# Performance work log

Hardware: AMD Instinct MI355X
Metric: run time of the kernel (lower is better)

## Reference

```python
import jax, jax.numpy as jnp
import numpy as np
import math

N = 50000       # nodes
E = 800000      # edges
C_IN = 64
C_OUT = 32
N_SH = 9        # (l_max+1)^2 with l_max=2
H = 32          # radial_hidden_dim


def spherical_harmonics(vectors):
    # vectors: [..., 3] -> [..., 9]; faithful to source incl. (x+iy).real == x
    norm = jnp.clip(jnp.linalg.norm(vectors, axis=-1, keepdims=True), 1e-8)
    d = vectors / norm
    x, y, z = d[..., 0], d[..., 1], d[..., 2]
    c00 = 0.5 / math.sqrt(math.pi)
    c1 = 0.5 * math.sqrt(3.0 / (2.0 * math.pi))
    c1z = 0.5 * math.sqrt(3.0 / math.pi)
    c2 = 0.25 * math.sqrt(15.0 / (2.0 * math.pi))
    c2z = 0.5 * math.sqrt(15.0 / (2.0 * math.pi))
    c20 = 0.25 * math.sqrt(5.0 / math.pi)
    feats = [
        c00 * jnp.ones_like(x),
        -c1 * x,                      # -0.5*sqrt(3/2pi)*(x+iy).real
        c1z * z,
        c1 * x,                       # 0.5*sqrt(3/2pi)*(x-iy).real
        c2 * (x * x - y * y),         # 0.25*sqrt(15/2pi)*((x+iy)^2).real
        -c2z * z * x,
        c20 * (2.0 * z * z - x * x - y * y),
        c2z * z * x,
        c2 * (x * x - y * y),
    ]
    return jnp.stack(feats, axis=-1)


def setup_inputs() -> dict:
    key = jax.random.key(0)
    ks = jax.random.split(key, 9)
    features = jax.random.normal(ks[0], (N, C_IN), dtype=jnp.float32)
    positions = jax.random.normal(ks[1], (N, 3), dtype=jnp.float32)
    edge_index = jax.random.randint(ks[2], (2, E), 0, N, dtype=jnp.int64)
    fan1 = N_SH + C_IN  # 73 (intended fan-in of first radial layer)
    W1 = jax.random.normal(ks[3], (fan1, H), dtype=jnp.float32) / math.sqrt(fan1)
    b1 = jnp.zeros((H,), dtype=jnp.float32)
    W2 = jax.random.normal(ks[4], (H, H), dtype=jnp.float32) / math.sqrt(H)
    b2 = jnp.zeros((H,), dtype=jnp.float32)
    W3 = jax.random.normal(ks[5], (H, N_SH * C_OUT), dtype=jnp.float32) / math.sqrt(H)
    b3 = jnp.zeros((N_SH * C_OUT,), dtype=jnp.float32)
    return {"features": features, "positions": positions, "W1": W1, "b1": b1,
            "W2": W2, "b2": b2, "W3": W3, "b3": b3, "edge_index": edge_index}


def reference(features, positions, W1, b1, W2, b2, W3, b3, edge_index):
    row, col = edge_index[0], edge_index[1]
    rel_pos = positions[row] - positions[col]                 # [E,3]
    dist = jnp.clip(jnp.linalg.norm(rel_pos, axis=-1, keepdims=True), 1e-8)
    directions = rel_pos / dist
    y_ij = spherical_harmonics(directions)                    # [E,9]
    combined = jnp.concatenate([y_ij, features[col]], axis=-1)  # [E,9+C_IN]
    h = jax.nn.silu(combined @ W1 + b1)
    h = jax.nn.silu(h @ W2 + b2)
    messages = h @ W3 + b3                                    # [E,9*C_OUT]
    msg = messages.reshape(-1, N_SH, C_OUT).sum(axis=1)       # [E,C_OUT]
    out = jax.ops.segment_sum(msg, row, num_segments=features.shape[0])
    return out
```

## Files before the change

kernel.cpp:

```cpp
#include <hip/hip_runtime.h>
#include <hip/hip_fp16.h>

#define NNODES 50000
#define NEDGES 800000
#define CIN 64
#define COUT 32
#define NSH 9
#define HDIM 32

#define NT_BLOCKS 6250
#define HIST_BLOCKS 782
#define SCAN_BLOCKS 125
#define SCAN_CHUNK 400

__device__ __forceinline__ void prep_body(
    int t, const float* __restrict__ W3, const float* __restrict__ b3,
    const float* __restrict__ W1, const float* __restrict__ b1,
    float* __restrict__ W3s, float* __restrict__ b3s, float* __restrict__ prm)
{
    if (t < HDIM * COUT) {
        int k = t >> 5, c = t & 31;
        float s = 0.f;
        #pragma unroll
        for (int q = 0; q < NSH; ++q) s += W3[k * (NSH * COUT) + q * COUT + c];
        W3s[t] = s;
    }
    if (t < COUT) {
        float s = 0.f;
        #pragma unroll
        for (int q = 0; q < NSH; ++q) s += b3[q * COUT + t];
        b3s[t] = s;
    }
    if (t < HDIM) {
        const float c00 = 0.28209479177387814f;
        const float c1  = 0.3454941494713355f;
        const float c1z = 0.4886025119029199f;
        const float c2  = 0.38627420202318958f;
        const float c2z = 0.7725484040463791f;
        const float c20 = 0.31539156525252005f;
        prm[t]       = b1[t] + c00 * W1[0 * HDIM + t];
        prm[32 + t]  = c1  * (W1[3 * HDIM + t] - W1[1 * HDIM + t]);
        prm[64 + t]  = c1z *  W1[2 * HDIM + t];
        prm[96 + t]  = c2z * (W1[7 * HDIM + t] - W1[5 * HDIM + t]);
        prm[128 + t] = c2  * (W1[4 * HDIM + t] + W1[8 * HDIM + t]);
        prm[160 + t] = c20 *  W1[6 * HDIM + t];
    }
}

__global__ void prep_w3(const float* __restrict__ W3, const float* __restrict__ b3,
                        const float* __restrict__ W1, const float* __restrict__ b1,
                        float* __restrict__ W3s, float* __restrict__ b3s,
                        float* __restrict__ prm) {
    prep_body(threadIdx.x, W3, b3, W1, b1, W3s, b3s, prm);
}

__global__ __launch_bounds__(256) void nt_hist(
    const float* __restrict__ feat, const float* __restrict__ W1,
    const int* __restrict__ ei, float* __restrict__ g1,
    int* __restrict__ cnt, int do_nt)
{
    int b = blockIdx.x;
    if (do_nt && b < NT_BLOCKS) {
        int tid = b * 256 + threadIdx.x;
        int n = tid >> 5, c = tid & 31;
        if (n < NNODES) {
            float acc = 0.f;
            const float* fr = feat + (size_t)n * CIN;
            const float* wp = W1 + NSH * HDIM + c;
            #pragma unroll 8
            for (int k = 0; k < CIN; ++k)
                acc = fmaf(fr[k], wp[k * HDIM], acc);
            g1[(size_t)n * HDIM + c] = acc;
        }
    } else {
        int hb = do_nt ? (b - NT_BLOCKS) : b;
        int e4 = (hb * 256 + threadIdx.x) * 4;
        if (e4 < NEDGES) {
            int4 r = *reinterpret_cast<const int4*>(ei + e4);
            atomicAdd(&cnt[r.x], 1);
            atomicAdd(&cnt[r.y], 1);
            atomicAdd(&cnt[r.z], 1);
            atomicAdd(&cnt[r.w], 1);
        }
    }
}

__global__ __launch_bounds__(256) void scan_bsum(const int* __restrict__ cnt,
                                                 int* __restrict__ bsum) {
    int b = blockIdx.x, t = threadIdx.x;
    int base = b * SCAN_CHUNK;
    int s = 0;
    for (int i = t; i < SCAN_CHUNK; i += 256) s += cnt[base + i];
    #pragma unroll
    for (int d = 32; d > 0; d >>= 1) s += __shfl_down(s, d);
    __shared__ int l4[4];
    if ((t & 63) == 0) l4[t >> 6] = s;
    __syncthreads();
    if (t == 0) bsum[b] = l4[0] + l4[1] + l4[2] + l4[3];
}

__global__ __launch_bounds__(1024) void scan_top_prep(
    const int* __restrict__ bsum, int* __restrict__ ebsum, int* __restrict__ off,
    const float* __restrict__ W3, const float* __restrict__ b3,
    const float* __restrict__ W1, const float* __restrict__ b1,
    float* __restrict__ W3s, float* __restrict__ b3s, float* __restrict__ prm)
{
    if (blockIdx.x == 1) {
        prep_body(threadIdx.x, W3, b3, W1, b1, W3s, b3s, prm);
        return;
    }
    __shared__ int lds[128];
    int t = threadIdx.x;
    if (t < 128) lds[t] = (t < SCAN_BLOCKS) ? bsum[t] : 0;
    __syncthreads();
    for (int d = 1; d < 128; d <<= 1) {
        int u = (t >= d && t < 128) ? lds[t - d] : 0;
        __syncthreads();
        if (t < 128) lds[t] += u;
        __syncthreads();
    }
    if (t < SCAN_BLOCKS) ebsum[t] = (t == 0) ? 0 : lds[t - 1];
    if (t == 0) off[NNODES] = NEDGES;
}

__global__ __launch_bounds__(256) void scan_offsets(const int* __restrict__ cnt,
                                                    const int* __restrict__ ebsum,
                                                    int* __restrict__ off,
                                                    int* __restrict__ cursor) {
    int b = blockIdx.x, t = threadIdx.x;
    int base = b * SCAN_CHUNK;
    __shared__ int lds[256];
    int2 c2 = make_int2(0, 0);
    if (t < SCAN_CHUNK / 2) c2 = reinterpret_cast<const int2*>(cnt + base)[t];
    int ps = c2.x + c2.y;
    lds[t] = ps;
    __syncthreads();
    for (int d = 1; d < 256; d <<= 1) {
        int u = (t >= d) ? lds[t - d] : 0;
        __syncthreads();
        lds[t] += u;
        __syncthreads();
    }
    int excl = lds[t] - ps;
    if (t < SCAN_CHUNK / 2) {
        int o = ebsum[b] + excl;
        int2 w = make_int2(o, o + c2.x);
        reinterpret_cast<int2*>(off + base)[t] = w;
        reinterpret_cast<int2*>(cursor + base)[t] = w;
    }
}

__global__ __launch_bounds__(256) void edge_compute_g1(
    const float* __restrict__ g1, const float* __restrict__ pos,
    const float* __restrict__ prm,
    const float* __restrict__ W2, const float* __restrict__ b2,
    const float* __restrict__ W3s, const float* __restrict__ b3s,
    const int* __restrict__ ei, int* __restrict__ cursor,
    unsigned int* __restrict__ msg)
{
    int e = blockIdx.x * blockDim.x + threadIdx.x;
    if (e >= NEDGES) return;
    int row = ei[e];
    int col = ei[NEDGES + e];

    int slot = atomicAdd(&cursor[row], 1);
    unsigned int* mp = msg + (size_t)slot * 16;

    float px = pos[3 * row + 0] - pos[3 * col + 0];
    float py = pos[3 * row + 1] - pos[3 * col + 1];
    float pz = pos[3 * row + 2] - pos[3 * col + 2];
    float dist = fmaxf(sqrtf(px * px + py * py + pz * pz), 1e-8f);
    float inv = 1.0f / dist;
    float dx = px * inv, dy = py * inv, dz = pz * inv;
    float n2 = fmaxf(sqrtf(dx * dx + dy * dy + dz * dz), 1e-8f);
    float i2 = 1.0f / n2;
    float x = dx * i2, y = dy * i2, z = dz * i2;

    float zx = z * x;
    float xxyy = x * x - y * y;
    float w6 = 2.f * z * z - x * x - y * y;

    const float* b1e = prm;
    const float* A = prm + 32;
    const float* B = prm + 64;
    const float* C = prm + 96;
    const float* D = prm + 128;
    const float* E = prm + 160;

    float h1[HDIM];
    const float4* g4 = reinterpret_cast<const float4*>(g1 + (size_t)col * HDIM);
    #pragma unroll
    for (int q = 0; q < 8; ++q) {
        float4 g = g4[q];
        h1[4 * q + 0] = g.x; h1[4 * q + 1] = g.y;
        h1[4 * q + 2] = g.z; h1[4 * q + 3] = g.w;
    }
    #pragma unroll
    for (int c = 0; c < HDIM; ++c) {
        float v = h1[c] + b1e[c];
        v = fmaf(x, A[c], v);
        v = fmaf(z, B[c], v);
        v = fmaf(zx, C[c], v);
        v = fmaf(xxyy, D[c], v);
        v = fmaf(w6, E[c], v);
        h1[c] = v / (1.f + __expf(-v));
    }

    float h2[HDIM];
    #pragma unroll
    for (int c = 0; c < HDIM; ++c) h2[c] = b2[c];
    for (int k = 0; k < HDIM; ++k) {
        float v = h1[k];
        #pragma unroll
        for (int c = 0; c < HDIM; ++c) h2[c] = fmaf(v, W2[k * HDIM + c], h2[c]);
    }
    #pragma unroll
    for (int c = 0; c < HDIM; ++c) {
        float v = h2[c];
        h2[c] = v / (1.f + __expf(-v));
    }

    float m[COUT];
    #pragma unroll
    for (int c = 0; c < COUT; ++c) m[c] = b3s[c];
    for (int k = 0; k < HDIM; ++k) {
        float v = h2[k];
        #pragma unroll
        for (int c = 0; c < COUT; ++c) m[c] = fmaf(v, W3s[k * COUT + c], m[c]);
    }

    uint4 pk[4];
    unsigned int* pu = reinterpret_cast<unsigned int*>(pk);
    #pragma unroll
    for (int q = 0; q < 16; ++q) {
        __half2 hh = __floats2half2_rn(m[2 * q], m[2 * q + 1]);
        pu[q] = *reinterpret_cast<unsigned int*>(&hh);
    }
    uint4* mp4 = reinterpret_cast<uint4*>(mp);
    #pragma unroll
    for (int q = 0; q < 4; ++q) mp4[q] = pk[q];
}

__global__ __launch_bounds__(256) void gather_kernel(
    const unsigned int* __restrict__ msg, const int* __restrict__ off,
    float* __restrict__ out)
{
    int node = blockIdx.x * 4 + (threadIdx.x >> 6);
    if (node >= NNODES) return;
    int lane = threadIdx.x & 63;
    int g = lane >> 4, p = lane & 15;
    int s0 = off[node], s1 = off[node + 1];
    float ax = 0.f, ay = 0.f;
    for (int s = s0 + g; s < s1; s += 4) {
        unsigned int u = msg[(size_t)s * 16 + p];
        __half2 h = *reinterpret_cast<__half2*>(&u);
        ax += __low2float(h);
        ay += __high2float(h);
    }
    ax += __shfl_xor(ax, 16); ay += __shfl_xor(ay, 16);
    ax += __shfl_xor(ax, 32); ay += __shfl_xor(ay, 32);
    if (lane < 16)
        reinterpret_cast<float2*>(out + (size_t)node * COUT)[p] = make_float2(ax, ay);
}

__global__ __launch_bounds__(256) void edge_atomic_kernel(
    const float* __restrict__ feat, const float* __restrict__ pos,
    const float* __restrict__ W1, const float* __restrict__ b1,
    const float* __restrict__ W2, const float* __restrict__ b2,
    const float* __restrict__ W3s, const float* __restrict__ b3s,
    const int* __restrict__ ei, float* __restrict__ out)
{
    int e = blockIdx.x * blockDim.x + threadIdx.x;
    if (e >= NEDGES) return;
    int row = ei[e];
    int col = ei[NEDGES + e];

    float px = pos[3 * row + 0] - pos[3 * col + 0];
    float py = pos[3 * row + 1] - pos[3 * col + 1];
    float pz = pos[3 * row + 2] - pos[3 * col + 2];
    float dist = fmaxf(sqrtf(px * px + py * py + pz * pz), 1e-8f);
    float inv = 1.0f / dist;
    float dx = px * inv, dy = py * inv, dz = pz * inv;
    float n2 = fmaxf(sqrtf(dx * dx + dy * dy + dz * dz), 1e-8f);
    float i2 = 1.0f / n2;
    float x = dx * i2, y = dy * i2, z = dz * i2;

    const float c00 = 0.28209479177387814f;
    const float c1  = 0.3454941494713355f;
    const float c1z = 0.4886025119029199f;
    const float c2  = 0.38627420202318958f;
    const float c2z = 0.7725484040463791f;
    const float c20 = 0.31539156525252005f;

    float sh[NSH];
    float xxyy = x * x - y * y;
    float zx = z * x;
    sh[0] = c00;
    sh[1] = -c1 * x;
    sh[2] = c1z * z;
    sh[3] = c1 * x;
    sh[4] = c2 * xxyy;
    sh[5] = -c2z * zx;
    sh[6] = c20 * (2.f * z * z - x * x - y * y);
    sh[7] = c2z * zx;
    sh[8] = c2 * xxyy;

    float h1[HDIM];
    #pragma unroll
    for (int c = 0; c < HDIM; ++c) h1[c] = b1[c];
    #pragma unroll
    for (int k = 0; k < NSH; ++k) {
        float v = sh[k];
        #pragma unroll
        for (int c = 0; c < HDIM; ++c) h1[c] = fmaf(v, W1[k * HDIM + c], h1[c]);
    }
    const float4* f4 = reinterpret_cast<const float4*>(feat + (size_t)col * CIN);
    for (int kk = 0; kk < CIN / 4; ++kk) {
        float4 f = f4[kk];
        const float* Wp = W1 + (NSH + kk * 4) * HDIM;
        #pragma unroll
        for (int c = 0; c < HDIM; ++c) h1[c] = fmaf(f.x, Wp[c], h1[c]);
        #pragma unroll
        for (int c = 0; c < HDIM; ++c) h1[c] = fmaf(f.y, Wp[HDIM + c], h1[c]);
        #pragma unroll
        for (int c = 0; c < HDIM; ++c) h1[c] = fmaf(f.z, Wp[2 * HDIM + c], h1[c]);
        #pragma unroll
        for (int c = 0; c < HDIM; ++c) h1[c] = fmaf(f.w, Wp[3 * HDIM + c], h1[c]);
    }
    #pragma unroll
    for (int c = 0; c < HDIM; ++c) {
        float v = h1[c];
        h1[c] = v / (1.f + __expf(-v));
    }

    float h2[HDIM];
    #pragma unroll
    for (int c = 0; c < HDIM; ++c) h2[c] = b2[c];
    for (int k = 0; k < HDIM; ++k) {
        float v = h1[k];
        #pragma unroll
        for (int c = 0; c < HDIM; ++c) h2[c] = fmaf(v, W2[k * HDIM + c], h2[c]);
    }
    #pragma unroll
    for (int c = 0; c < HDIM; ++c) {
        float v = h2[c];
        h2[c] = v / (1.f + __expf(-v));
    }

    float m[COUT];
    #pragma unroll
    for (int c = 0; c < COUT; ++c) m[c] = b3s[c];
    for (int k = 0; k < HDIM; ++k) {
        float v = h2[k];
        #pragma unroll
        for (int c = 0; c < COUT; ++c) m[c] = fmaf(v, W3s[k * COUT + c], m[c]);
    }

    float* op = out + (size_t)row * COUT;
    #pragma unroll
    for (int c = 0; c < COUT; ++c) atomicAdd(op + c, m[c]);
}

extern "C" void kernel_launch(void* const* d_in, const int* in_sizes, int n_in,
                              void* d_out, int out_size, void* d_ws, size_t ws_size,
                              hipStream_t stream) {
    const float* feat = (const float*)d_in[0];
    const float* pos  = (const float*)d_in[1];
    const float* W1   = (const float*)d_in[2];
    const float* b1   = (const float*)d_in[3];
    const float* W2   = (const float*)d_in[4];
    const float* b2   = (const float*)d_in[5];
    const float* W3   = (const float*)d_in[6];
    const float* b3   = (const float*)d_in[7];
    const int*   ei   = (const int*)d_in[8];
    float* outf = (float*)d_out;

    int* cnt    = (int*)d_ws;
    int* off    = cnt + NNODES;
    int* cursor = off + NNODES + 2;
    int* bsum   = cursor + NNODES;
    int* ebsum  = bsum + 128;
    const size_t head_ints = ((size_t)NNODES + (NNODES + 2) + NNODES + 128 + 128 + 3) & ~(size_t)3;
    float* fbase = (float*)(((int*)d_ws) + head_ints);
    float* W3s = fbase;
    float* b3s = W3s + HDIM * COUT;
    float* prm = b3s + COUT;
    const size_t head_floats = HDIM * COUT + COUT + 192;
    float* g1 = fbase + head_floats;
    unsigned int* msg = (unsigned int*)(g1 + (size_t)NNODES * HDIM);
    size_t need = (head_ints + head_floats + (size_t)NNODES * HDIM) * 4
                + (size_t)NEDGES * 16 * 4;

    if (ws_size >= need) {
        (void)hipMemsetAsync(cnt, 0, (size_t)NNODES * sizeof(int), stream);
        nt_hist<<<NT_BLOCKS + HIST_BLOCKS, 256, 0, stream>>>(feat, W1, ei, g1, cnt, 1);
        scan_bsum<<<SCAN_BLOCKS, 256, 0, stream>>>(cnt, bsum);
        scan_top_prep<<<2, 1024, 0, stream>>>(bsum, ebsum, off, W3, b3, W1, b1, W3s, b3s, prm);
        scan_offsets<<<SCAN_BLOCKS, 256, 0, stream>>>(cnt, ebsum, off, cursor);
        edge_compute_g1<<<(NEDGES + 255) / 256, 256, 0, stream>>>(
            g1, pos, prm, W2, b2, W3s, b3s, ei, cursor, msg);
        gather_kernel<<<(NNODES + 3) / 4, 256, 0, stream>>>(msg, off, outf);
    } else {
        (void)hipMemsetAsync(d_out, 0, (size_t)out_size * sizeof(float), stream);
        prep_w3<<<1, 1024, 0, stream>>>(W3, b3, W1, b1, W3s, b3s, prm);
        edge_atomic_kernel<<<(NEDGES + 255) / 256, 256, 0, stream>>>(
            feat, pos, W1, b1, W2, b2, W3s, b3s, ei, outf);
    }
}
```

Measured before the change: 160.8 us.

## Store node projection in fp16, merge scan kernels, use fast rsqrt and silu

The per-node first-layer projection is now stored as half precision, which halves the gather traffic per edge in the edge kernel. The three-kernel prefix scan is replaced by a single block that does a serial per-thread chunk scan plus an LDS scan, cutting two launches. The double normalisation becomes one hardware rsqrt, and silu uses the hardware reciprocal. These trade some precision (fp16 storage, approximate rcp and rsq) for less memory traffic and fewer ALU ops, and the serial scan in one block may be slow because its per-thread cnt reads are strided and uncoalesced.

Result: slower. 251.4 us (+56.4%).

```diff
diff --git a/kernel.cpp b/kernel.cpp
--- a/kernel.cpp
+++ b/kernel.cpp
@@ -10,8 +10,6 @@
 
 #define NT_BLOCKS 6250
 #define HIST_BLOCKS 782
-#define SCAN_BLOCKS 125
-#define SCAN_CHUNK 400
 
 __device__ __forceinline__ void prep_body(
     int t, const float* __restrict__ W3, const float* __restrict__ b3,
@@ -56,7 +54,7 @@
 
 __global__ __launch_bounds__(256) void nt_hist(
     const float* __restrict__ feat, const float* __restrict__ W1,
-    const int* __restrict__ ei, float* __restrict__ g1,
+    const int* __restrict__ ei, __half* __restrict__ g1h,
     int* __restrict__ cnt, int do_nt)
 {
     int b = blockIdx.x;
@@ -70,7 +68,7 @@
             #pragma unroll 8
             for (int k = 0; k < CIN; ++k)
                 acc = fmaf(fr[k], wp[k * HDIM], acc);
-            g1[(size_t)n * HDIM + c] = acc;
+            g1h[(size_t)n * HDIM + c] = __float2half(acc);
         }
     } else {
         int hb = do_nt ? (b - NT_BLOCKS) : b;
@@ -85,22 +83,8 @@
     }
 }
 
-__global__ __launch_bounds__(256) void scan_bsum(const int* __restrict__ cnt,
-                                                 int* __restrict__ bsum) {
-    int b = blockIdx.x, t = threadIdx.x;
-    int base = b * SCAN_CHUNK;
-    int s = 0;
-    for (int i = t; i < SCAN_CHUNK; i += 256) s += cnt[base + i];
-    #pragma unroll
-    for (int d = 32; d > 0; d >>= 1) s += __shfl_down(s, d);
-    __shared__ int l4[4];
-    if ((t & 63) == 0) l4[t >> 6] = s;
-    __syncthreads();
-    if (t == 0) bsum[b] = l4[0] + l4[1] + l4[2] + l4[3];
-}
-
-__global__ __launch_bounds__(1024) void scan_top_prep(
-    const int* __restrict__ bsum, int* __restrict__ ebsum, int* __restrict__ off,
+__global__ __launch_bounds__(1024) void scan_all(
+    const int* __restrict__ cnt, int* __restrict__ off, int* __restrict__ cursor,
     const float* __restrict__ W3, const float* __restrict__ b3,
     const float* __restrict__ W1, const float* __restrict__ b1,
     float* __restrict__ W3s, float* __restrict__ b3s, float* __restrict__ prm)
@@ -109,49 +93,35 @@
         prep_body(threadIdx.x, W3, b3, W1, b1, W3s, b3s, prm);
         return;
     }
-    __shared__ int lds[128];
+    __shared__ int lds[1024];
+    const int C = (NNODES + 1023) / 1024;
     int t = threadIdx.x;
-    if (t < 128) lds[t] = (t < SCAN_BLOCKS) ? bsum[t] : 0;
+    int begin = t * C, end = min(begin + C, NNODES);
+    int s = 0;
+    for (int i = begin; i < end; ++i) s += cnt[i];
+    lds[t] = s;
     __syncthreads();
-    for (int d = 1; d < 128; d <<= 1) {
-        int u = (t >= d && t < 128) ? lds[t - d] : 0;
+    for (int d = 1; d < 1024; d <<= 1) {
+        int v = (t >= d) ? lds[t - d] : 0;
         __syncthreads();
-        if (t < 128) lds[t] += u;
+        lds[t] += v;
         __syncthreads();
     }
-    if (t < SCAN_BLOCKS) ebsum[t] = (t == 0) ? 0 : lds[t - 1];
-    if (t == 0) off[NNODES] = NEDGES;
-}
-
-__global__ __launch_bounds__(256) void scan_offsets(const int* __restrict__ cnt,
-                                                    const int* __restrict__ ebsum,
-                                                    int* __restrict__ off,
-                                                    int* __restrict__ cursor) {
-    int b = blockIdx.x, t = threadIdx.x;
-    int base = b * SCAN_CHUNK;
-    __shared__ int lds[256];
-    int2 c2 = make_int2(0, 0);
-    if (t < SCAN_CHUNK / 2) c2 = reinterpret_cast<const int2*>(cnt + base)[t];
-    int ps = c2.x + c2.y;
-    lds[t] = ps;
-    __syncthreads();
-    for (int d = 1; d < 256; d <<= 1) {
-        int u = (t >= d) ? lds[t - d] : 0;
-        __syncthreads();
-        lds[t] += u;
-        __syncthreads();
-    }
-    int excl = lds[t] - ps;
-    if (t < SCAN_CHUNK / 2) {
-        int o = ebsum[b] + excl;
-        int2 w = make_int2(o, o + c2.x);
-        reinterpret_cast<int2*>(off + base)[t] = w;
-        reinterpret_cast<int2*>(cursor + base)[t] = w;
-    }
+    int base = (t == 0) ? 0 : lds[t - 1];
+    for (int i = begin; i < end; ++i) {
+        off[i] = base;
+        cursor[i] = base;
+        base += cnt[i];
+    }
+    if (t == 1023) off[NNODES] = lds[1023];
+}
+
+__device__ __forceinline__ float fast_silu(float v) {
+    return v * __builtin_amdgcn_rcpf(1.f + __expf(-v));
 }
 
 __global__ __launch_bounds__(256) void edge_compute_g1(
-    const float* __restrict__ g1, const float* __restrict__ pos,
+    const __half* __restrict__ g1h, const float* __restrict__ pos,
     const float* __restrict__ prm,
     const float* __restrict__ W2, const float* __restrict__ b2,
     const float* __restrict__ W3s, const float* __restrict__ b3s,
@@ -169,12 +139,9 @@
     float px = pos[3 * row + 0] - pos[3 * col + 0];
     float py = pos[3 * row + 1] - pos[3 * col + 1];
     float pz = pos[3 * row + 2] - pos[3 * col + 2];
-    float dist = fmaxf(sqrtf(px * px + py * py + pz * pz), 1e-8f);
-    float inv = 1.0f / dist;
-    float dx = px * inv, dy = py * inv, dz = pz * inv;
-    float n2 = fmaxf(sqrtf(dx * dx + dy * dy + dz * dz), 1e-8f);
-    float i2 = 1.0f / n2;
-    float x = dx * i2, y = dy * i2, z = dz * i2;
+    float r2 = px * px + py * py + pz * pz;
+    float rs = (r2 >= 1e-16f) ? __builtin_amdgcn_rsqf(r2) : 0.f;
+    float x = px * rs, y = py * rs, z = pz * rs;
 
     float zx = z * x;
     float xxyy = x * x - y * y;
@@ -188,12 +155,17 @@
     const float* E = prm + 160;
 
     float h1[HDIM];
-    const float4* g4 = reinterpret_cast<const float4*>(g1 + (size_t)col * HDIM);
-    #pragma unroll
-    for (int q = 0; q < 8; ++q) {
-        float4 g = g4[q];
-        h1[4 * q + 0] = g.x; h1[4 * q + 1] = g.y;
-        h1[4 * q + 2] = g.z; h1[4 * q + 3] = g.w;
+    const uint4* g4 = reinterpret_cast<const uint4*>(g1h + (size_t)col * HDIM);
+    #pragma unroll
+    for (int q = 0; q < 4; ++q) {
+        uint4 u = g4[q];
+        const unsigned int uw[4] = {u.x, u.y, u.z, u.w};
+        #pragma unroll
+        for (int j = 0; j < 4; ++j) {
+            float2 f = __half22float2(*reinterpret_cast<const __half2*>(&uw[j]));
+            h1[8 * q + 2 * j]     = f.x;
+            h1[8 * q + 2 * j + 1] = f.y;
+        }
     }
     #pragma unroll
     for (int c = 0; c < HDIM; ++c) {
@@ -203,7 +175,7 @@
         v = fmaf(zx, C[c], v);
         v = fmaf(xxyy, D[c], v);
         v = fmaf(w6, E[c], v);
-        h1[c] = v / (1.f + __expf(-v));
+        h1[c] = fast_silu(v);
     }
 
     float h2[HDIM];
@@ -215,10 +187,7 @@
         for (int c = 0; c < HDIM; ++c) h2[c] = fmaf(v, W2[k * HDIM + c], h2[c]);
     }
     #pragma unroll
-    for (int c = 0; c < HDIM; ++c) {
-        float v = h2[c];
-        h2[c] = v / (1.f + __expf(-v));
-    }
+    for (int c = 0; c < HDIM; ++c) h2[c] = fast_silu(h2[c]);
 
     float m[COUT];
     #pragma unroll
@@ -278,12 +247,9 @@
     float px = pos[3 * row + 0] - pos[3 * col + 0];
     float py = pos[3 * row + 1] - pos[3 * col + 1];
     float pz = pos[3 * row + 2] - pos[3 * col + 2];
-    float dist = fmaxf(sqrtf(px * px + py * py + pz * pz), 1e-8f);
-    float inv = 1.0f / dist;
-    float dx = px * inv, dy = py * inv, dz = pz * inv;
-    float n2 = fmaxf(sqrtf(dx * dx + dy * dy + dz * dz), 1e-8f);
-    float i2 = 1.0f / n2;
-    float x = dx * i2, y = dy * i2, z = dz * i2;
+    float r2 = px * px + py * py + pz * pz;
+    float rs = (r2 >= 1e-16f) ? __builtin_amdgcn_rsqf(r2) : 0.f;
+    float x = px * rs, y = py * rs, z = pz * rs;
 
     const float c00 = 0.28209479177387814f;
     const float c1  = 0.3454941494713355f;
@@ -328,10 +294,7 @@
         for (int c = 0; c < HDIM; ++c) h1[c] = fmaf(f.w, Wp[3 * HDIM + c], h1[c]);
     }
     #pragma unroll
-    for (int c = 0; c < HDIM; ++c) {
-        float v = h1[c];
-        h1[c] = v / (1.f + __expf(-v));
-    }
+    for (int c = 0; c < HDIM; ++c) h1[c] = fast_silu(h1[c]);
 
     float h2[HDIM];
     #pragma unroll
@@ -342,10 +305,7 @@
         for (int c = 0; c < HDIM; ++c) h2[c] = fmaf(v, W2[k * HDIM + c], h2[c]);
     }
     #pragma unroll
-    for (int c = 0; c < HDIM; ++c) {
-        float v = h2[c];
-        h2[c] = v / (1.f + __expf(-v));
-    }
+    for (int c = 0; c < HDIM; ++c) h2[c] = fast_silu(h2[c]);
 
     float m[COUT];
     #pragma unroll
@@ -378,27 +338,24 @@
     int* cnt    = (int*)d_ws;
     int* off    = cnt + NNODES;
     int* cursor = off + NNODES + 2;
-    int* bsum   = cursor + NNODES;
-    int* ebsum  = bsum + 128;
-    const size_t head_ints = ((size_t)NNODES + (NNODES + 2) + NNODES + 128 + 128 + 3) & ~(size_t)3;
+    const size_t head_ints = ((size_t)NNODES + (NNODES + 2) + NNODES + 3) & ~(size_t)3;
     float* fbase = (float*)(((int*)d_ws) + head_ints);
     float* W3s = fbase;
     float* b3s = W3s + HDIM * COUT;
     float* prm = b3s + COUT;
     const size_t head_floats = HDIM * COUT + COUT + 192;
-    float* g1 = fbase + head_floats;
-    unsigned int* msg = (unsigned int*)(g1 + (size_t)NNODES * HDIM);
-    size_t need = (head_ints + head_floats + (size_t)NNODES * HDIM) * 4
-                + (size_t)NEDGES * 16 * 4;
+    __half* g1h = (__half*)(fbase + head_floats);
+    unsigned int* msg = (unsigned int*)(g1h + (size_t)NNODES * HDIM);
+    size_t need = (head_ints + head_floats) * 4
+                + (size_t)NNODES * HDIM * 2
+                + (size_t)NEDGES * 64;
 
     if (ws_size >= need) {
         (void)hipMemsetAsync(cnt, 0, (size_t)NNODES * sizeof(int), stream);
-        nt_hist<<<NT_BLOCKS + HIST_BLOCKS, 256, 0, stream>>>(feat, W1, ei, g1, cnt, 1);
-        scan_bsum<<<SCAN_BLOCKS, 256, 0, stream>>>(cnt, bsum);
-        scan_top_prep<<<2, 1024, 0, stream>>>(bsum, ebsum, off, W3, b3, W1, b1, W3s, b3s, prm);
-        scan_offsets<<<SCAN_BLOCKS, 256, 0, stream>>>(cnt, ebsum, off, cursor);
+        nt_hist<<<NT_BLOCKS + HIST_BLOCKS, 256, 0, stream>>>(feat, W1, ei, g1h, cnt, 1);
+        scan_all<<<2, 1024, 0, stream>>>(cnt, off, cursor, W3, b3, W1, b1, W3s, b3s, prm);
         edge_compute_g1<<<(NEDGES + 255) / 256, 256, 0, stream>>>(
-            g1, pos, prm, W2, b2, W3s, b3s, ei, cursor, msg);
+            g1h, pos, prm, W2, b2, W3s, b3s, ei, cursor, msg);
         gather_kernel<<<(NNODES + 3) / 4, 256, 0, stream>>>(msg, off, outf);
     } else {
         (void)hipMemsetAsync(d_out, 0, (size_t)out_size * sizeof(float), stream);
```
